# Performance work log

Measured on AMD Instinct MI355X. Metric: run time of the kernel, lower is better.

Reference implementation:

```python
import jax, jax.numpy as jnp
import numpy as np

VOCAB = 10000
EMB = 512
D_IMG = 2048
RNN = 1024
SEQ_LEN = 16
START_TOKEN = VOCAB + 1  # 10001
V_OUT = VOCAB + 3        # 10003


def setup_inputs() -> dict:
    key = jax.random.key(0)
    ks = jax.random.split(key, 24)
    g = lambda k, shape, fan_in: jax.random.normal(k, shape, jnp.float32) / np.sqrt(fan_in)
    inp = {
        "img_features": jax.random.normal(ks[0], (64, 196, D_IMG), jnp.float32),
        "captions": jax.random.randint(ks[1], (64, SEQ_LEN), 0, VOCAB),
        # embedding table
        "emb": g(ks[2], (V_OUT, EMB), EMB),
        # LSTMCell (PyTorch gate order i,f,g,o), stored as [in, 4H]
        "Wih": g(ks[3], (EMB + D_IMG, 4 * RNN), EMB + D_IMG),
        "Whh": g(ks[4], (RNN, 4 * RNN), RNN),
        "bih": jnp.zeros((4 * RNN,), jnp.float32),
        "bhh": jnp.zeros((4 * RNN,), jnp.float32),
        # init_h / init_c
        "Wh0": g(ks[5], (D_IMG, RNN), D_IMG), "bh0": jnp.zeros((RNN,), jnp.float32),
        "Wc0": g(ks[6], (D_IMG, RNN), D_IMG), "bc0": jnp.zeros((RNN,), jnp.float32),
        # f_beta gate
        "Wfb": g(ks[7], (RNN, D_IMG), RNN), "bfb": jnp.zeros((D_IMG,), jnp.float32),
        # deep_output
        "Wout": g(ks[8], (RNN, V_OUT), RNN), "bout": jnp.zeros((V_OUT,), jnp.float32),
        # attention: U (rnn->rnn), W (img->rnn), v (rnn->1)
        "WU": g(ks[9], (RNN, RNN), RNN), "bU": jnp.zeros((RNN,), jnp.float32),
        "WW": g(ks[10], (D_IMG, RNN), D_IMG), "bW": jnp.zeros((RNN,), jnp.float32),
        "Wv": g(ks[11], (RNN, 1), RNN), "bv": jnp.zeros((1,), jnp.float32),
    }
    return inp


def reference(img_features, captions, emb, Wih, Whh, bih, bhh, Wh0, bh0, Wc0, bc0,
              Wfb, bfb, Wout, bout, WU, bU, WW, bW, Wv, bv):
    B = img_features.shape[0]
    # get_target: prepend START token -> [B, T+1]
    start = jnp.full((B, 1), START_TOKEN, dtype=captions.dtype)
    target = jnp.concatenate([start, captions], axis=1)
    embedding = emb[target]                      # [B, T+1, EMB]
    emb_seq = jnp.transpose(embedding, (1, 0, 2))  # [T+1, B, EMB]

    # init LSTM state from mean image features
    avg = img_features.mean(axis=1)              # [B, D_IMG]
    h0 = jnp.tanh(avg @ Wh0 + bh0)
    c0 = jnp.tanh(avg @ Wc0 + bc0)

    # image-side attention projection is timestep-independent
    W_s = img_features @ WW + bW                 # [B, L, RNN]
    b_gates = bih + bhh

    def step(carry, emb_t):
        h, c = carry
        # additive attention
        U_h = h @ WU + bU                        # [B, RNN]
        att = jnp.tanh(W_s + U_h[:, None, :])    # [B, L, RNN]
        e = (att @ Wv).squeeze(-1) + bv          # [B, L]
        alpha = jax.nn.softmax(e, axis=1)
        context = jnp.einsum('bld,bl->bd', img_features, alpha)  # [B, D_IMG]
        gate = jax.nn.sigmoid(h @ Wfb + bfb)
        x = jnp.concatenate([emb_t, gate * context], axis=1)     # [B, EMB+D_IMG]
        # LSTMCell, PyTorch gate order i,f,g,o
        gates = x @ Wih + h @ Whh + b_gates      # [B, 4*RNN]
        i, f, gg, o = jnp.split(gates, 4, axis=1)
        c_new = jax.nn.sigmoid(f) * c + jax.nn.sigmoid(i) * jnp.tanh(gg)
        h_new = jax.nn.sigmoid(o) * jnp.tanh(c_new)
        out = h_new @ Wout + bout                # [B, V_OUT] (dropout=identity, eval mode)
        return (h_new, c_new), (out, alpha)

    (_, _), (preds_t, alphas_t) = jax.lax.scan(step, (h0, c0), emb_seq)
    preds = jnp.transpose(preds_t, (1, 0, 2))    # [B, T+1, V_OUT]
    alphas = jnp.transpose(alphas_t, (1, 0, 2))  # [B, T+1, L]
    return preds, alphas
```

## Files before the change

### kernel.cpp

```cpp
#include <hip/hip_runtime.h>
#include <cstdint>

#define NB    64
#define LIMG  196
#define DIMG  2048
#define RNND  1024
#define EMBD  512
#define TSTEPS 17
#define VOUTD 10003

typedef short bf16x8 __attribute__((ext_vector_type(8)));
typedef float f32x4  __attribute__((ext_vector_type(4)));

__device__ __forceinline__ float fast_sig(float x) {
    return 1.f / (1.f + __expf(-x));
}
__device__ __forceinline__ float fast_tanh(float x) {
    float ax = fabsf(x);
    float e  = __expf(2.f * ax);
    float r  = 1.f - 2.f / (e + 1.f);
    return copysignf(r, x);
}
__device__ __forceinline__ void split_bf(float x, short& hi, short& lo) {
    unsigned u  = __float_as_uint(x);
    unsigned hb = u & 0xffff0000u;
    hi = (short)(u >> 16);
    float r = x - __uint_as_float(hb);
    lo = (short)(__float_as_uint(r) >> 16);
}

__global__ __launch_bounds__(256) void tsplit(
    const float* __restrict__ S1, int ld1,
    const float* __restrict__ S2, int ld2,
    short* __restrict__ outh, short* __restrict__ outl,
    int N, int K, int ksplit, int nsplit)
{
    __shared__ float T[64][65];
    const int k0 = blockIdx.x * 64, n0 = blockIdx.y * 64;
    const int tid = threadIdx.x;
    const int rr = tid >> 2;
    const int cc = (tid & 3) * 16;
    const int kk = k0 + rr;
    const int nn = n0 + cc;
    const float* rp; int col;
    if (nsplit > 0) {
        if (nn >= nsplit) { rp = S2 + (size_t)kk * ld2; col = nn - nsplit; }
        else              { rp = S1 + (size_t)kk * ld1; col = nn; }
    } else {
        if (kk < ksplit)  { rp = S1 + (size_t)kk * ld1; col = nn; }
        else              { rp = S2 + (size_t)(kk - ksplit) * ld2; col = nn; }
    }
#pragma unroll
    for (int j = 0; j < 16; j++)
        T[rr][cc + j] = (nn + j < N) ? rp[col + j] : 0.f;
    __syncthreads();
    const int wn = tid >> 2;
    const int wk = (tid & 3) * 16;
    const int gn = n0 + wn;
    if (gn >= N) return;
    bf16x8 h0, h1, l0, l1;
#pragma unroll
    for (int j = 0; j < 8; j++) {
        short hh, ll;
        split_bf(T[wk + j][wn], hh, ll);     h0[j] = hh; l0[j] = ll;
        split_bf(T[wk + 8 + j][wn], hh, ll); h1[j] = hh; l1[j] = ll;
    }
    const size_t o = (size_t)gn * K + k0 + wk;
    *(bf16x8*)&outh[o]     = h0;
    *(bf16x8*)&outh[o + 8] = h1;
    *(bf16x8*)&outl[o]     = l0;
    *(bf16x8*)&outl[o + 8] = l1;
}

__global__ __launch_bounds__(256) void gemm_bb(
    const float* __restrict__ Af,
    const short* __restrict__ Ah16, const short* __restrict__ Al16,
    const short* __restrict__ Bh16, const short* __restrict__ Bl16,
    const float* __restrict__ bias, float* __restrict__ C,
    int M, int N, int K, int lda, int ldb, int ldc, int pmap)
{
    __shared__ short Ah[128 * 40], Al[128 * 40];
    __shared__ short Bh[128 * 40], Bl[128 * 40];

    const int tid = threadIdx.x;
    const int n0  = blockIdx.x * 128;
    const int m0  = blockIdx.y * 128;

    const int lane = tid & 63;
    const int w    = tid >> 6;
    const int wm   = (w >> 1) * 64;
    const int wn   = (w & 1) * 64;
    const int lm   = lane & 15;
    const int lk   = lane >> 4;

    const int ar = tid >> 1;
    const int ac = (tid & 1) * 16;

    f32x4 acc[4][4];
#pragma unroll
    for (int i = 0; i < 4; i++)
#pragma unroll
        for (int j = 0; j < 4; j++) acc[i][j] = (f32x4)0.f;

    for (int k0 = 0; k0 < K; k0 += 32) {
        bf16x8 ah0, ah1, al0, al1;
        if (Af) {
            float f[16];
            if (m0 + ar < M) {
                const float* ap = Af + (size_t)(m0 + ar) * lda + (k0 + ac);
                float4 q0 = *(const float4*)(ap);
                float4 q1 = *(const float4*)(ap + 4);
                float4 q2 = *(const float4*)(ap + 8);
                float4 q3 = *(const float4*)(ap + 12);
                f[0]=q0.x; f[1]=q0.y; f[2]=q0.z; f[3]=q0.w;
                f[4]=q1.x; f[5]=q1.y; f[6]=q1.z; f[7]=q1.w;
                f[8]=q2.x; f[9]=q2.y; f[10]=q2.z; f[11]=q2.w;
                f[12]=q3.x; f[13]=q3.y; f[14]=q3.z; f[15]=q3.w;
            } else {
#pragma unroll
                for (int j = 0; j < 16; j++) f[j] = 0.f;
            }
#pragma unroll
            for (int j = 0; j < 8; j++) {
                short hh, ll;
                split_bf(f[j], hh, ll);     ah0[j] = hh; al0[j] = ll;
                split_bf(f[8 + j], hh, ll); ah1[j] = hh; al1[j] = ll;
            }
        } else {
            const short* p = Ah16 + (size_t)(m0 + ar) * lda + (k0 + ac);
            ah0 = *(const bf16x8*)p; ah1 = *(const bf16x8*)(p + 8);
            const short* q = Al16 + (size_t)(m0 + ar) * lda + (k0 + ac);
            al0 = *(const bf16x8*)q; al1 = *(const bf16x8*)(q + 8);
        }
        const short* pb = Bh16 + (size_t)(n0 + ar) * ldb + (k0 + ac);
        bf16x8 bh0 = *(const bf16x8*)pb, bh1 = *(const bf16x8*)(pb + 8);
        const short* qb = Bl16 + (size_t)(n0 + ar) * ldb + (k0 + ac);
        bf16x8 bl0 = *(const bf16x8*)qb, bl1 = *(const bf16x8*)(qb + 8);

        __syncthreads();
        *(bf16x8*)&Ah[ar * 40 + ac]     = ah0;
        *(bf16x8*)&Ah[ar * 40 + ac + 8] = ah1;
        *(bf16x8*)&Al[ar * 40 + ac]     = al0;
        *(bf16x8*)&Al[ar * 40 + ac + 8] = al1;
        *(bf16x8*)&Bh[ar * 40 + ac]     = bh0;
        *(bf16x8*)&Bh[ar * 40 + ac + 8] = bh1;
        *(bf16x8*)&Bl[ar * 40 + ac]     = bl0;
        *(bf16x8*)&Bl[ar * 40 + ac + 8] = bl1;
        __syncthreads();

        bf16x8 afh[4], afl[4], bfh[4], bfl[4];
#pragma unroll
        for (int fm = 0; fm < 4; fm++) {
            const int idx = (wm + fm * 16 + lm) * 40 + lk * 8;
            afh[fm] = *(bf16x8*)&Ah[idx];
            afl[fm] = *(bf16x8*)&Al[idx];
        }
#pragma unroll
        for (int fn = 0; fn < 4; fn++) {
            const int idx = (wn + fn * 16 + lm) * 40 + lk * 8;
            bfh[fn] = *(bf16x8*)&Bh[idx];
            bfl[fn] = *(bf16x8*)&Bl[idx];
        }
#pragma unroll
        for (int fm = 0; fm < 4; fm++)
#pragma unroll
            for (int fn = 0; fn < 4; fn++) {
                acc[fm][fn] = __builtin_amdgcn_mfma_f32_16x16x32_bf16(afh[fm], bfh[fn], acc[fm][fn], 0, 0, 0);
                acc[fm][fn] = __builtin_amdgcn_mfma_f32_16x16x32_bf16(afh[fm], bfl[fn], acc[fm][fn], 0, 0, 0);
                acc[fm][fn] = __builtin_amdgcn_mfma_f32_16x16x32_bf16(afl[fm], bfh[fn], acc[fm][fn], 0, 0, 0);
            }
    }

#pragma unroll
    for (int fm = 0; fm < 4; fm++) {
#pragma unroll
        for (int fn = 0; fn < 4; fn++) {
            const int col = n0 + wn + fn * 16 + lm;
            if (col >= N) continue;
            const float bb = bias ? bias[col] : 0.f;
#pragma unroll
            for (int r = 0; r < 4; r++) {
                const int row = m0 + wm + fm * 16 + lk * 4 + r;
                if (row >= M) continue;
                const size_t orow = pmap ? (size_t)((row & 63) * TSTEPS + (row >> 6))
                                         : (size_t)row;
                C[orow * ldc + col] = acc[fm][fn][r] + bb;
            }
        }
    }
}

__global__ __launch_bounds__(256) void gemm_sk(
    const float* __restrict__ A,
    const short* __restrict__ Bh16, const short* __restrict__ Bl16,
    float* __restrict__ P, int N, int K, int lda, int ldb, int Kc)
{
    __shared__ short Ah[64 * 40], Al[64 * 40];
    __shared__ short Bh[128 * 40], Bl[128 * 40];

    const int tid = threadIdx.x;
    const int n0  = blockIdx.x * 128;
    const int s   = blockIdx.z;
    const int kb  = s * Kc;

    const int lane = tid & 63;
    const int w    = tid >> 6;
    const int wn   = w * 32;
    const int lm   = lane & 15;
    const int lk   = lane >> 4;

    const int a_r = tid >> 2;
    const int a_c = (tid & 3) * 8;
    const int b_r = tid >> 1;
    const int b_c = (tid & 1) * 16;

    f32x4 acc[4][2];
#pragma unroll
    for (int i = 0; i < 4; i++)
#pragma unroll
        for (int j = 0; j < 2; j++) acc[i][j] = (f32x4)0.f;

    for (int k0 = kb; k0 < kb + Kc; k0 += 32) {
        const float* ap = A + (size_t)a_r * lda + (k0 + a_c);
        float4 q0 = *(const float4*)(ap);
        float4 q1 = *(const float4*)(ap + 4);
        float f[8] = {q0.x, q0.y, q0.z, q0.w, q1.x, q1.y, q1.z, q1.w};
        bf16x8 ah, al;
#pragma unroll
        for (int j = 0; j < 8; j++) {
            short hh, ll;
            split_bf(f[j], hh, ll); ah[j] = hh; al[j] = ll;
        }
        const short* pb = Bh16 + (size_t)(n0 + b_r) * ldb + (k0 + b_c);
        bf16x8 bh0 = *(const bf16x8*)pb, bh1 = *(const bf16x8*)(pb + 8);
        const short* qb = Bl16 + (size_t)(n0 + b_r) * ldb + (k0 + b_c);
        bf16x8 bl0 = *(const bf16x8*)qb, bl1 = *(const bf16x8*)(qb + 8);

        __syncthreads();
        *(bf16x8*)&Ah[a_r * 40 + a_c] = ah;
        *(bf16x8*)&Al[a_r * 40 + a_c] = al;
        *(bf16x8*)&Bh[b_r * 40 + b_c]     = bh0;
        *(bf16x8*)&Bh[b_r * 40 + b_c + 8] = bh1;
        *(bf16x8*)&Bl[b_r * 40 + b_c]     = bl0;
        *(bf16x8*)&Bl[b_r * 40 + b_c + 8] = bl1;
        __syncthreads();

        bf16x8 afh[4], afl[4], bfh[2], bfl[2];
#pragma unroll
        for (int fm = 0; fm < 4; fm++) {
            const int idx = (fm * 16 + lm) * 40 + lk * 8;
            afh[fm] = *(bf16x8*)&Ah[idx];
            afl[fm] = *(bf16x8*)&Al[idx];
        }
#pragma unroll
        for (int fn = 0; fn < 2; fn++) {
            const int idx = (wn + fn * 16 + lm) * 40 + lk * 8;
            bfh[fn] = *(bf16x8*)&Bh[idx];
            bfl[fn] = *(bf16x8*)&Bl[idx];
        }
#pragma unroll
        for (int fm = 0; fm < 4; fm++)
#pragma unroll
            for (int fn = 0; fn < 2; fn++) {
                acc[fm][fn] = __builtin_amdgcn_mfma_f32_16x16x32_bf16(afh[fm], bfh[fn], acc[fm][fn], 0, 0, 0);
                acc[fm][fn] = __builtin_amdgcn_mfma_f32_16x16x32_bf16(afh[fm], bfl[fn], acc[fm][fn], 0, 0, 0);
                acc[fm][fn] = __builtin_amdgcn_mfma_f32_16x16x32_bf16(afl[fm], bfh[fn], acc[fm][fn], 0, 0, 0);
            }
    }

    float* Ps = P + (size_t)s * 64 * N;
#pragma unroll
    for (int fm = 0; fm < 4; fm++)
#pragma unroll
        for (int fn = 0; fn < 2; fn++) {
            const int col = n0 + wn + fn * 16 + lm;
#pragma unroll
            for (int r = 0; r < 4; r++) {
                const int row = fm * 16 + lk * 4 + r;
                Ps[(size_t)row * N + col] = acc[fm][fn][r];
            }
        }
}

__global__ __launch_bounds__(256) void gemm64(
    const float* __restrict__ A, const float* __restrict__ B,
    const float* __restrict__ bias, float* __restrict__ C,
    int N, int K, int Kc, int ldc, int act, int direct)
{
    __shared__ float As[16][64];
    __shared__ float Bs[16][68];

    const int tid = threadIdx.x;
    const int n0  = blockIdx.x * 64;
    const int m0  = blockIdx.y * 64;
    const int s   = blockIdx.z;
    const int kb  = s * Kc;
    const int ke  = min(K, kb + Kc);

    const int tm = (tid >> 4) << 2;
    const int tn = (tid & 15) << 2;

    float acc[4][4];
#pragma unroll
    for (int i = 0; i < 4; i++)
#pragma unroll
        for (int j = 0; j < 4; j++) acc[i][j] = 0.f;

    const int a_m = tid >> 2;
    const int a_k = (tid & 3) << 2;
    const int b_k = tid >> 4;
    const int b_n = (tid & 15) << 2;
    const bool n4 = ((N & 3) == 0);

    for (int k0 = kb; k0 < ke; k0 += 16) {
        float4 av = *(const float4*)(A + (size_t)(m0 + a_m) * K + (k0 + a_k));
        float4 bv;
        {
            const int nn = n0 + b_n;
            const float* brow = B + (size_t)(k0 + b_k) * N;
            if (n4) {
                bv = (nn < N) ? *(const float4*)(brow + nn) : make_float4(0.f,0.f,0.f,0.f);
            } else {
                bv.x = (nn + 0 < N) ? brow[nn + 0] : 0.f;
                bv.y = (nn + 1 < N) ? brow[nn + 1] : 0.f;
                bv.z = (nn + 2 < N) ? brow[nn + 2] : 0.f;
                bv.w = (nn + 3 < N) ? brow[nn + 3] : 0.f;
            }
        }
        __syncthreads();
        As[a_k + 0][a_m] = av.x;
        As[a_k + 1][a_m] = av.y;
        As[a_k + 2][a_m] = av.z;
        As[a_k + 3][a_m] = av.w;
        *(float4*)&Bs[b_k][b_n] = bv;
        __syncthreads();
#pragma unroll
        for (int k = 0; k < 16; k++) {
            float4 a4 = *(const float4*)&As[k][tm];
            float4 b4 = *(const float4*)&Bs[k][tn];
            acc[0][0] = fmaf(a4.x, b4.x, acc[0][0]);
            acc[0][1] = fmaf(a4.x, b4.y, acc[0][1]);
            acc[0][2] = fmaf(a4.x, b4.z, acc[0][2]);
            acc[0][3] = fmaf(a4.x, b4.w, acc[0][3]);
            acc[1][0] = fmaf(a4.y, b4.x, acc[1][0]);
            acc[1][1] = fmaf(a4.y, b4.y, acc[1][1]);
            acc[1][2] = fmaf(a4.y, b4.z, acc[1][2]);
            acc[1][3] = fmaf(a4.y, b4.w, acc[1][3]);
            acc[2][0] = fmaf(a4.z, b4.x, acc[2][0]);
            acc[2][1] = fmaf(a4.z, b4.y, acc[2][1]);
            acc[2][2] = fmaf(a4.z, b4.z, acc[2][2]);
            acc[2][3] = fmaf(a4.z, b4.w, acc[2][3]);
            acc[3][0] = fmaf(a4.w, b4.x, acc[3][0]);
            acc[3][1] = fmaf(a4.w, b4.y, acc[3][1]);
            acc[3][2] = fmaf(a4.w, b4.z, acc[3][2]);
            acc[3][3] = fmaf(a4.w, b4.w, acc[3][3]);
        }
    }

    if (direct) {
#pragma unroll
        for (int i = 0; i < 4; i++) {
            const int m = m0 + tm + i;
            const size_t row = (size_t)m * ldc;
#pragma unroll
            for (int j = 0; j < 4; j++) {
                const int n = n0 + tn + j;
                if (n < N) {
                    float v = acc[i][j] + (bias ? bias[n] : 0.f);
                    if (act == 1) v = fast_tanh(v);
                    else if (act == 2) v = fast_sig(v);
                    C[row + n] = v;
                }
            }
        }
    } else {
        float* Pp = C + (size_t)s * 64 * N;
#pragma unroll
        for (int i = 0; i < 4; i++) {
#pragma unroll
            for (int j = 0; j < 4; j++) {
                const int n = n0 + tn + j;
                if (n < N) Pp[(size_t)(tm + i) * N + n] = acc[i][j];
            }
        }
    }
}

__global__ __launch_bounds__(256) void gemm_mfma3(
    const float* __restrict__ A, const float* __restrict__ B,
    const float* __restrict__ bias, float* __restrict__ C,
    int M, int N, int K, int lda, int ldb, int ldc, int pmap)
{
    __shared__ short Ah[128 * 40], Al[128 * 40];
    __shared__ short Bh[128 * 40], Bl[128 * 40];

    const int tid = threadIdx.x;
    const int n0  = blockIdx.x * 128;
    const int m0  = blockIdx.y * 128;

    const int lane = tid & 63;
    const int w    = tid >> 6;
    const int wm   = (w >> 1) * 64;
    const int wn   = (w & 1) * 64;
    const int lm   = lane & 15;
    const int lk   = lane >> 4;

    const int ar = tid >> 1;
    const int ac = (tid & 1) * 16;
    const int kb = (tid & 15) * 2;
    const int c8 = (tid >> 4) * 8;

    const bool bvec = ((ldb & 3) == 0) && (n0 + 128 <= N);

    f32x4 acc[4][4];
#pragma unroll
    for (int i = 0; i < 4; i++)
#pragma unroll
        for (int j = 0; j < 4; j++) acc[i][j] = (f32x4)0.f;

    for (int k0 = 0; k0 < K; k0 += 32) {
        float f[16];
        if (m0 + ar < M) {
            const float* ap = A + (size_t)(m0 + ar) * lda + (k0 + ac);
            float4 q0 = *(const float4*)(ap);
            float4 q1 = *(const float4*)(ap + 4);
            float4 q2 = *(const float4*)(ap + 8);
            float4 q3 = *(const float4*)(ap + 12);
            f[0]=q0.x; f[1]=q0.y; f[2]=q0.z; f[3]=q0.w;
            f[4]=q1.x; f[5]=q1.y; f[6]=q1.z; f[7]=q1.w;
            f[8]=q2.x; f[9]=q2.y; f[10]=q2.z; f[11]=q2.w;
            f[12]=q3.x; f[13]=q3.y; f[14]=q3.z; f[15]=q3.w;
        } else {
#pragma unroll
            for (int j = 0; j < 16; j++) f[j] = 0.f;
        }
        bf16x8 h0, h1, l0, l1;
#pragma unroll
        for (int j = 0; j < 8; j++) {
            short hh, ll;
            split_bf(f[j], hh, ll);     h0[j] = hh; l0[j] = ll;
            split_bf(f[8 + j], hh, ll); h1[j] = hh; l1[j] = ll;
        }
        float g0[8], g1[8];
        if (bvec) {
            const float* bp0 = B + (size_t)(k0 + kb) * ldb + (n0 + c8);
            const float* bp1 = bp0 + ldb;
            float4 q0 = *(const float4*)(bp0);
            float4 q1 = *(const float4*)(bp0 + 4);
            float4 q2 = *(const float4*)(bp1);
            float4 q3 = *(const float4*)(bp1 + 4);
            g0[0]=q0.x; g0[1]=q0.y; g0[2]=q0.z; g0[3]=q0.w;
            g0[4]=q1.x; g0[5]=q1.y; g0[6]=q1.z; g0[7]=q1.w;
            g1[0]=q2.x; g1[1]=q2.y; g1[2]=q2.z; g1[3]=q2.w;
            g1[4]=q3.x; g1[5]=q3.y; g1[6]=q3.z; g1[7]=q3.w;
        } else {
            const float* bp0 = B + (size_t)(k0 + kb) * ldb;
            const float* bp1 = bp0 + ldb;
#pragma unroll
            for (int j = 0; j < 8; j++) {
                const int nn = n0 + c8 + j;
                g0[j] = (nn < N) ? bp0[nn] : 0.f;
                g1[j] = (nn < N) ? bp1[nn] : 0.f;
            }
        }
        __syncthreads();
        *(bf16x8*)&Ah[ar * 40 + ac]     = h0;
        *(bf16x8*)&Ah[ar * 40 + ac + 8] = h1;
        *(bf16x8*)&Al[ar * 40 + ac]     = l0;
        *(bf16x8*)&Al[ar * 40 + ac + 8] = l1;
#pragma unroll
        for (int j = 0; j < 8; j++) {
            short ha, la, hb, lb;
            split_bf(g0[j], ha, la);
            split_bf(g1[j], hb, lb);
            const int ci = (c8 + j) * 40 + kb;
            *(int*)&Bh[ci] = (int)((unsigned short)ha | ((unsigned)(unsigned short)hb << 16));
            *(int*)&Bl[ci] = (int)((unsigned short)la | ((unsigned)(unsigned short)lb << 16));
        }
        __syncthreads();

        bf16x8 afh[4], afl[4], bfh[4], bfl[4];
#pragma unroll
        for (int fm = 0; fm < 4; fm++) {
            const int idx = (wm + fm * 16 + lm) * 40 + lk * 8;
            afh[fm] = *(bf16x8*)&Ah[idx];
            afl[fm] = *(bf16x8*)&Al[idx];
        }
#pragma unroll
        for (int fn = 0; fn < 4; fn++) {
            const int idx = (wn + fn * 16 + lm) * 40 + lk * 8;
            bfh[fn] = *(bf16x8*)&Bh[idx];
            bfl[fn] = *(bf16x8*)&Bl[idx];
        }
#pragma unroll
        for (int fm = 0; fm < 4; fm++)
#pragma unroll
            for (int fn = 0; fn < 4; fn++) {
                acc[fm][fn] = __builtin_amdgcn_mfma_f32_16x16x32_bf16(afh[fm], bfh[fn], acc[fm][fn], 0, 0, 0);
                acc[fm][fn] = __builtin_amdgcn_mfma_f32_16x16x32_bf16(afh[fm], bfl[fn], acc[fm][fn], 0, 0, 0);
                acc[fm][fn] = __builtin_amdgcn_mfma_f32_16x16x32_bf16(afl[fm], bfh[fn], acc[fm][fn], 0, 0, 0);
            }
    }

#pragma unroll
    for (int fm = 0; fm < 4; fm++) {
#pragma unroll
        for (int fn = 0; fn < 4; fn++) {
            const int col = n0 + wn + fn * 16 + lm;
            if (col >= N) continue;
            const float bb = bias ? bias[col] : 0.f;
#pragma unroll
            for (int r = 0; r < 4; r++) {
                const int row = m0 + wm + fm * 16 + lk * 4 + r;
                if (row >= M) continue;
                const size_t orow = pmap ? (size_t)((row & 63) * TSTEPS + (row >> 6))
                                         : (size_t)row;
                C[orow * ldc + col] = acc[fm][fn][r] + bb;
            }
        }
    }
}

__global__ __launch_bounds__(256) void reduce_partials(
    const float* __restrict__ P, int S, int N,
    const float* __restrict__ bias, float* __restrict__ C, int ldc, int act)
{
    const int idx = blockIdx.x * 256 + threadIdx.x;
    const int total = 64 * N;
    if (idx >= total) return;
    const int m = idx / N;
    const int n = idx - m * N;
    float v = bias ? bias[n] : 0.f;
    for (int s = 0; s < S; s++) v += P[(size_t)s * total + idx];
    if (act == 1) v = fast_tanh(v);
    else if (act == 2) v = fast_sig(v);
    else if (act == 3 && n >= RNND) v = fast_sig(v);
    C[(size_t)m * ldc + n] = v;
}

__global__ __launch_bounds__(256) void reduce_lstm(
    const float* __restrict__ P, int S, const float* __restrict__ bsum,
    float* __restrict__ hn, float* __restrict__ c,
    short* __restrict__ hbh, short* __restrict__ hbl)
{
    const int idx = blockIdx.x * 256 + threadIdx.x;
    const int b = idx >> 10, r = idx & 1023;
    const float* pb = P + (size_t)b * 4096;
    float gi = bsum[r], gf = bsum[1024 + r], gg = bsum[2048 + r], go = bsum[3072 + r];
    for (int s = 0; s < S; s++) {
        const float* q = pb + (size_t)s * 64 * 4096;
        gi += q[r]; gf += q[1024 + r]; gg += q[2048 + r]; go += q[3072 + r];
    }
    const float ig = fast_sig(gi);
    const float fg = fast_sig(gf);
    const float g2 = fast_tanh(gg);
    const float og = fast_sig(go);
    const float cn = fg * c[idx] + ig * g2;
    const float hv = og * fast_tanh(cn);
    c[idx]  = cn;
    hn[idx] = hv;
    if (hbh) {
        short hi, lo;
        split_bf(hv, hi, lo);
        hbh[idx] = hi;
        hbl[idx] = lo;
    }
}

__global__ __launch_bounds__(256) void mean_img(
    const float* __restrict__ img, float* __restrict__ avg)
{
    const int b = blockIdx.x;
    const int d = blockIdx.y * 256 + threadIdx.x;
    const float* p = img + (size_t)b * LIMG * DIMG + d;
    float s = 0.f;
    for (int l = 0; l < LIMG; l++) s += p[(size_t)l * DIMG];
    avg[(size_t)b * DIMG + d] = s * (1.f / 196.f);
}

__global__ __launch_bounds__(256) void concat_w(
    const float* __restrict__ WU, const float* __restrict__ Wfb,
    float* __restrict__ Wug)
{
    const int idx = blockIdx.x * 256 + threadIdx.x;
    if (idx >= 1024 * 3072) return;
    const int k = idx / 3072;
    const int j = idx - k * 3072;
    Wug[idx] = (j < 1024) ? WU[(size_t)k * 1024 + j] : Wfb[(size_t)k * 2048 + (j - 1024)];
}

__global__ __launch_bounds__(256) void concat_b(
    const float* __restrict__ bU, const float* __restrict__ bfb,
    const float* __restrict__ bih, const float* __restrict__ bhh,
    float* __restrict__ bug, float* __restrict__ bsum)
{
    const int j = blockIdx.x * 256 + threadIdx.x;
    if (j < 3072) bug[j] = (j < 1024) ? bU[j] : bfb[j - 1024];
    if (j < 4096) bsum[j] = bih[j] + bhh[j];
}

__global__ __launch_bounds__(256) void attn_e(
    const float* __restrict__ Ws, const float* __restrict__ ug,
    const float* __restrict__ Wv, const float* __restrict__ bv,
    float* __restrict__ e)
{
    const int wv   = (blockIdx.x << 2) + (threadIdx.x >> 6);
    const int lane = threadIdx.x & 63;
    const int b    = wv / LIMG;
    const float* wrow = Ws + (size_t)wv * RNND;
    const float* urow = ug + (size_t)b * 3072;
    float acc = 0.f;
#pragma unroll
    for (int k = lane * 4; k < RNND; k += 256) {
        float4 wq = *(const float4*)(wrow + k);
        float4 uq = *(const float4*)(urow + k);
        float4 vq = *(const float4*)(Wv + k);
        acc += fast_tanh(wq.x + uq.x) * vq.x + fast_tanh(wq.y + uq.y) * vq.y
             + fast_tanh(wq.z + uq.z) * vq.z + fast_tanh(wq.w + uq.w) * vq.w;
    }
#pragma unroll
    for (int off = 32; off > 0; off >>= 1) acc += __shfl_down(acc, off);
    if (lane == 0) e[wv] = acc + bv[0];
}

__global__ __launch_bounds__(256) void softmax_alpha(
    const float* __restrict__ e, float* __restrict__ alpha,
    float* __restrict__ alphas_out, int t)
{
    __shared__ float red[256];
    const int b = blockIdx.x, tid = threadIdx.x;
    const float v = (tid < LIMG) ? e[b * LIMG + tid] : -3.0e38f;
    red[tid] = v; __syncthreads();
    for (int s = 128; s > 0; s >>= 1) {
        if (tid < s) red[tid] = fmaxf(red[tid], red[tid + s]);
        __syncthreads();
    }
    const float mx = red[0]; __syncthreads();
    const float ex = (tid < LIMG) ? __expf(v - mx) : 0.f;
    red[tid] = ex; __syncthreads();
    for (int s = 128; s > 0; s >>= 1) {
        if (tid < s) red[tid] += red[tid + s];
        __syncthreads();
    }
    const float inv = 1.f / red[0];
    if (tid < LIMG) {
        const float a = ex * inv;
        alpha[b * LIMG + tid] = a;
        alphas_out[(size_t)b * (TSTEPS * LIMG) + t * LIMG + tid] = a;
    }
}

__global__ __launch_bounds__(128) void assemble_x(
    const float* __restrict__ img, const float* __restrict__ alpha,
    const float* __restrict__ ug, const float* __restrict__ emb,
    const int* __restrict__ captions, const float* __restrict__ h,
    float* __restrict__ x, int t, int stride)
{
    const int b = blockIdx.x, y = blockIdx.y, tid = threadIdx.x;
    if (y < 4) {
        const int tok = (t == 0) ? 10001 : captions[b * 16 + (t - 1)];
        const int j = y * 128 + tid;
        x[(size_t)b * stride + j] = emb[(size_t)tok * EMBD + j];
    } else if (y < 20) {
        __shared__ float al[LIMG];
        for (int i = tid; i < LIMG; i += 128) al[i] = alpha[b * LIMG + i];
        __syncthreads();
        const int d = (y - 4) * 128 + tid;
        const float* ib = img + (size_t)b * LIMG * DIMG + d;
        float accv = 0.f;
#pragma unroll 4
        for (int l = 0; l < LIMG; l++) accv = fmaf(al[l], ib[(size_t)l * DIMG], accv);
        const float g = ug[(size_t)b * 3072 + 1024 + d];
        x[(size_t)b * stride + EMBD + d] = g * accv;
    } else {
        const int j = (y - 20) * 128 + tid;
        x[(size_t)b * stride + 2560 + j] = h[(size_t)b * RNND + j];
    }
}

extern "C" void kernel_launch(void* const* d_in, const int* in_sizes, int n_in,
                              void* d_out, int out_size, void* d_ws, size_t ws_size,
                              hipStream_t stream)
{
    const float* img      = (const float*)d_in[0];
    const int*   captions = (const int*)d_in[1];
    const float* emb      = (const float*)d_in[2];
    const float* Wih      = (const float*)d_in[3];
    const float* Whh      = (const float*)d_in[4];
    const float* bih      = (const float*)d_in[5];
    const float* bhh      = (const float*)d_in[6];
    const float* Wh0      = (const float*)d_in[7];
    const float* bh0      = (const float*)d_in[8];
    const float* Wc0      = (const float*)d_in[9];
    const float* bc0      = (const float*)d_in[10];
    const float* Wfb      = (const float*)d_in[11];
    const float* bfb      = (const float*)d_in[12];
    const float* Wout     = (const float*)d_in[13];
    const float* bout     = (const float*)d_in[14];
    const float* WU       = (const float*)d_in[15];
    const float* bU       = (const float*)d_in[16];
    const float* WW       = (const float*)d_in[17];
    const float* bW       = (const float*)d_in[18];
    const float* Wv       = (const float*)d_in[19];
    const float* bv       = (const float*)d_in[20];

    float* preds      = (float*)d_out;
    float* alphas_out = preds + (size_t)NB * TSTEPS * VOUTD;

    const size_t NEED = 190000000;

    if (ws_size >= NEED) {
        float* w = (float*)d_ws;
        float* Ws    = w; w += (size_t)12544 * 1024;
        float* ug    = w; w += (size_t)64 * 3072;
        float* P     = w; w += (size_t)8 * 64 * 4096;
        float* e     = w; w += (size_t)64 * LIMG;
        float* alpha = w; w += (size_t)64 * LIMG;
        float* xh    = w; w += (size_t)64 * 3584;
        float* h     = w; w += (size_t)64 * RNND;
        float* c     = w; w += (size_t)64 * RNND;
        float* avg   = w; w += (size_t)64 * DIMG;
        float* bsum  = w; w += 4096;
        float* bug   = w; w += 3072;
        short* u = (short*)w;
        short* Hbh     = u; u += (size_t)1280 * 1024;
        short* Hbl     = u; u += (size_t)1280 * 1024;
        short* WWTh    = u; u += (size_t)1024 * 2048;
        short* WWTl    = u; u += (size_t)1024 * 2048;
        short* WugTh   = u; u += (size_t)3072 * 1024;
        short* WugTl   = u; u += (size_t)3072 * 1024;
        short* WfullTh = u; u += (size_t)4096 * 3584;
        short* WfullTl = u; u += (size_t)4096 * 3584;
        short* WoutTh  = u; u += (size_t)10112 * 1024;
        short* WoutTl  = u; u += (size_t)10112 * 1024;

        mean_img<<<dim3(NB, 8), 256, 0, stream>>>(img, avg);
        gemm64<<<dim3(16, 1, 8), 256, 0, stream>>>(avg, Wh0, nullptr, P, 1024, 2048, 256, 0, 0, 0);
        reduce_partials<<<256, 256, 0, stream>>>(P, 8, 1024, bh0, h, 1024, 1);
        gemm64<<<dim3(16, 1, 8), 256, 0, stream>>>(avg, Wc0, nullptr, P, 1024, 2048, 256, 0, 0, 0);
        reduce_partials<<<256, 256, 0, stream>>>(P, 8, 1024, bc0, c, 1024, 1);
        concat_b<<<16, 256, 0, stream>>>(bU, bfb, bih, bhh, bug, bsum);

        tsplit<<<dim3(32, 16), 256, 0, stream>>>(WW, 1024, WW, 1024, WWTh, WWTl, 1024, 2048, 2048, 0);
        tsplit<<<dim3(16, 48), 256, 0, stream>>>(WU, 1024, Wfb, 2048, WugTh, WugTl, 3072, 1024, 1024, 1024);
        tsplit<<<dim3(56, 64), 256, 0, stream>>>(Wih, 4096, Whh, 4096, WfullTh, WfullTl, 4096, 3584, 2560, 0);
        tsplit<<<dim3(16, 157), 256, 0, stream>>>(Wout, VOUTD, Wout, VOUTD, WoutTh, WoutTl, VOUTD, 1024, 1024, 0);

        gemm_bb<<<dim3(8, 98), 256, 0, stream>>>(img, nullptr, nullptr, WWTh, WWTl,
                                                 bW, Ws, 12544, 1024, 2048, 2048, 2048, 1024, 0);

        for (int t = 0; t < TSTEPS; t++) {
            gemm_sk<<<dim3(24, 1, 8), 256, 0, stream>>>(h, WugTh, WugTl, P, 3072, 1024, 1024, 1024, 128);
            reduce_partials<<<768, 256, 0, stream>>>(P, 8, 3072, bug, ug, 3072, 3);
            attn_e<<<3136, 256, 0, stream>>>(Ws, ug, Wv, bv, e);
            softmax_alpha<<<NB, 256, 0, stream>>>(e, alpha, alphas_out, t);
            assemble_x<<<dim3(NB, 28), 128, 0, stream>>>(img, alpha, ug, emb, captions, h, xh, t, 3584);
            gemm_sk<<<dim3(32, 1, 7), 256, 0, stream>>>(xh, WfullTh, WfullTl, P, 4096, 3584, 3584, 3584, 512);
            reduce_lstm<<<256, 256, 0, stream>>>(P, 7, bsum, h, c,
                                                 Hbh + (size_t)(t + 1) * 65536,
                                                 Hbl + (size_t)(t + 1) * 65536);
        }

        gemm_bb<<<dim3(79, 9), 256, 0, stream>>>(nullptr, Hbh + 65536, Hbl + 65536,
                                                 WoutTh, WoutTl, bout, preds,
                                                 1088, VOUTD, 1024, 1024, 1024, VOUTD, 1);
    } else {
        float* w = (float*)d_ws;
        float* Ws    = w; w += (size_t)12544 * 1024;
        float* ug    = w; w += (size_t)64 * 3072;
        float* P     = w; w += (size_t)12 * 64 * 4096;
        float* e     = w; w += (size_t)64 * LIMG;
        float* alpha = w; w += (size_t)64 * LIMG;
        float* x     = w; w += (size_t)64 * 2560;
        float* Hh    = w; w += (size_t)18 * 64 * RNND;
        float* c     = w; w += (size_t)64 * RNND;
        float* avg   = w; w += (size_t)64 * DIMG;
        float* bsum  = w; w += 4096;
        float* Wug   = w; w += (size_t)1024 * 3072;
        float* bug   = w; w += 3072;

        mean_img<<<dim3(NB, 8), 256, 0, stream>>>(img, avg);
        gemm64<<<dim3(16, 1, 8), 256, 0, stream>>>(avg, Wh0, nullptr, P, 1024, 2048, 256, 0, 0, 0);
        reduce_partials<<<256, 256, 0, stream>>>(P, 8, 1024, bh0, Hh, 1024, 1);
        gemm64<<<dim3(16, 1, 8), 256, 0, stream>>>(avg, Wc0, nullptr, P, 1024, 2048, 256, 0, 0, 0);
        reduce_partials<<<256, 256, 0, stream>>>(P, 8, 1024, bc0, c, 1024, 1);
        concat_b<<<16, 256, 0, stream>>>(bU, bfb, bih, bhh, bug, bsum);
        concat_w<<<12288, 256, 0, stream>>>(WU, Wfb, Wug);
        gemm_mfma3<<<dim3(8, 98), 256, 0, stream>>>(img, WW, bW, Ws,
                                                    12544, 1024, 2048, 2048, 1024, 1024, 0);
        for (int t = 0; t < TSTEPS; t++) {
            const float* h  = Hh + (size_t)t * 64 * RNND;
            float*       hn = Hh + (size_t)(t + 1) * 64 * RNND;
            gemm64<<<dim3(48, 1, 8), 256, 0, stream>>>(h, Wug, nullptr, P, 3072, 1024, 128, 0, 0, 0);
            reduce_partials<<<768, 256, 0, stream>>>(P, 8, 3072, bug, ug, 3072, 3);
            attn_e<<<3136, 256, 0, stream>>>(Ws, ug, Wv, bv, e);
            softmax_alpha<<<NB, 256, 0, stream>>>(e, alpha, alphas_out, t);
            assemble_x<<<dim3(NB, 20), 128, 0, stream>>>(img, alpha, ug, emb, captions, h, x, t, 2560);
            gemm64<<<dim3(64, 1, 8), 256, 0, stream>>>(x, Wih, nullptr, P, 4096, 2560, 320, 0, 0, 0);
            gemm64<<<dim3(64, 1, 4), 256, 0, stream>>>(h, Whh, nullptr, P + (size_t)8 * 64 * 4096,
                                                       4096, 1024, 256, 0, 0, 0);
            reduce_lstm<<<256, 256, 0, stream>>>(P, 12, bsum, hn, c, nullptr, nullptr);
        }
        gemm_mfma3<<<dim3(79, 9), 256, 0, stream>>>(Hh + (size_t)64 * RNND, Wout, bout, preds,
                                                    TSTEPS * 64, VOUTD, 1024, 1024, VOUTD, VOUTD, 1);
    }
}
```

Before: 1.828 ms.

## Fuse softmax with context assembly and remap GEMM blocks per XCD

Merges the per-step softmax_alpha and assemble_x kernels into a single ctx_fuse kernel. Each block recomputes the softmax over 196 positions, then either writes alphas, the embedding and h, or computes a 512-wide slice of the gated context. This removes one launch per timestep. The bf16-split GEMM now takes a 1D grid that is remapped so contiguous tile groups land on the same XCD, aiming for better L2 reuse. The cost is redundant softmax work in every block and a lower-parallelism context kernel (5x64 blocks of 256 threads, versus 28x64 blocks of 128 before).

```diff
diff --git a/kernel.cpp b/kernel.cpp
--- a/kernel.cpp
+++ b/kernel.cpp
@@ -77,15 +77,27 @@
     const short* __restrict__ Ah16, const short* __restrict__ Al16,
     const short* __restrict__ Bh16, const short* __restrict__ Bl16,
     const float* __restrict__ bias, float* __restrict__ C,
-    int M, int N, int K, int lda, int ldb, int ldc, int pmap)
+    int M, int N, int K, int lda, int ldb, int ldc, int pmap,
+    int nx, int ny, int gax)
 {
     __shared__ short Ah[128 * 40], Al[128 * 40];
     __shared__ short Bh[128 * 40], Bl[128 * 40];
 
+    const int p    = blockIdx.x;
+    const int xcd  = p & 7;
+    const int slot = p >> 3;
+    const int G = gax ? ny : nx;
+    const int O = gax ? nx : ny;
+    const int qb = G >> 3, qr = G & 7;
+    const int cnt = qb + (xcd < qr ? 1 : 0);
+    if (slot >= cnt * O) return;
+    const int start = xcd * qb + min(xcd, qr);
+    const int g = start + slot / O;
+    const int o = slot - (slot / O) * O;
+    const int n0 = (gax ? o : g) * 128;
+    const int m0 = (gax ? g : o) * 128;
+
     const int tid = threadIdx.x;
-    const int n0  = blockIdx.x * 128;
-    const int m0  = blockIdx.y * 128;
-
     const int lane = tid & 63;
     const int w    = tid >> 6;
     const int wm   = (w >> 1) * 64;
@@ -127,15 +139,15 @@
                 split_bf(f[8 + j], hh, ll); ah1[j] = hh; al1[j] = ll;
             }
         } else {
-            const short* p = Ah16 + (size_t)(m0 + ar) * lda + (k0 + ac);
-            ah0 = *(const bf16x8*)p; ah1 = *(const bf16x8*)(p + 8);
-            const short* q = Al16 + (size_t)(m0 + ar) * lda + (k0 + ac);
-            al0 = *(const bf16x8*)q; al1 = *(const bf16x8*)(q + 8);
+            const short* pa = Ah16 + (size_t)(m0 + ar) * lda + (k0 + ac);
+            ah0 = *(const bf16x8*)pa; ah1 = *(const bf16x8*)(pa + 8);
+            const short* qa = Al16 + (size_t)(m0 + ar) * lda + (k0 + ac);
+            al0 = *(const bf16x8*)qa; al1 = *(const bf16x8*)(qa + 8);
         }
         const short* pb = Bh16 + (size_t)(n0 + ar) * ldb + (k0 + ac);
         bf16x8 bh0 = *(const bf16x8*)pb, bh1 = *(const bf16x8*)(pb + 8);
-        const short* qb = Bl16 + (size_t)(n0 + ar) * ldb + (k0 + ac);
-        bf16x8 bl0 = *(const bf16x8*)qb, bl1 = *(const bf16x8*)(qb + 8);
+        const short* qb2 = Bl16 + (size_t)(n0 + ar) * ldb + (k0 + ac);
+        bf16x8 bl0 = *(const bf16x8*)qb2, bl1 = *(const bf16x8*)(qb2 + 8);
 
         __syncthreads();
         *(bf16x8*)&Ah[ar * 40 + ac]     = ah0;
@@ -621,6 +633,58 @@
 #pragma unroll
     for (int off = 32; off > 0; off >>= 1) acc += __shfl_down(acc, off);
     if (lane == 0) e[wv] = acc + bv[0];
+}
+
+__global__ __launch_bounds__(256) void ctx_fuse(
+    const float* __restrict__ e, const float* __restrict__ img,
+    const float* __restrict__ ug, const float* __restrict__ embt,
+    const int* __restrict__ captions, const float* __restrict__ h,
+    float* __restrict__ x, float* __restrict__ alphas_out, int t)
+{
+    __shared__ float al[256];
+    __shared__ float red[256];
+    const int b = blockIdx.x, y = blockIdx.y, tid = threadIdx.x;
+
+    const float v = (tid < LIMG) ? e[b * LIMG + tid] : -3.0e38f;
+    red[tid] = v; __syncthreads();
+    for (int s = 128; s > 0; s >>= 1) {
+        if (tid < s) red[tid] = fmaxf(red[tid], red[tid + s]);
+        __syncthreads();
+    }
+    const float mx = red[0]; __syncthreads();
+    const float ex = (tid < LIMG) ? __expf(v - mx) : 0.f;
+    red[tid] = ex; __syncthreads();
+    for (int s = 128; s > 0; s >>= 1) {
+        if (tid < s) red[tid] += red[tid + s];
+        __syncthreads();
+    }
+    const float inv = 1.f / red[0];
+    al[tid] = ex * inv;
+    __syncthreads();
+
+    if (y == 0) {
+        if (tid < LIMG)
+            alphas_out[(size_t)b * (TSTEPS * LIMG) + t * LIMG + tid] = al[tid];
+        const int tok = (t == 0) ? 10001 : captions[b * 16 + (t - 1)];
+        for (int j = tid; j < EMBD; j += 256)
+            x[(size_t)b * 3584 + j] = embt[(size_t)tok * EMBD + j];
+        for (int j = tid; j < RNND; j += 256)
+            x[(size_t)b * 3584 + 2560 + j] = h[(size_t)b * RNND + j];
+    } else {
+        const int d0 = (y - 1) * 512 + tid * 2;
+        const float* ib = img + (size_t)b * LIMG * DIMG + d0;
+        float a0 = 0.f, a1 = 0.f;
+#pragma unroll 4
+        for (int l = 0; l < LIMG; l++) {
+            float2 q = *(const float2*)(ib + (size_t)l * DIMG);
+            a0 = fmaf(al[l], q.x, a0);
+            a1 = fmaf(al[l], q.y, a1);
+        }
+        const float g0 = ug[(size_t)b * 3072 + 1024 + d0];
+        const float g1 = ug[(size_t)b * 3072 + 1024 + d0 + 1];
+        x[(size_t)b * 3584 + EMBD + d0]     = g0 * a0;
+        x[(size_t)b * 3584 + EMBD + d0 + 1] = g1 * a1;
+    }
 }
 
 __global__ __launch_bounds__(256) void softmax_alpha(
@@ -746,24 +810,25 @@
         tsplit<<<dim3(56, 64), 256, 0, stream>>>(Wih, 4096, Whh, 4096, WfullTh, WfullTl, 4096, 3584, 2560, 0);
         tsplit<<<dim3(16, 157), 256, 0, stream>>>(Wout, VOUTD, Wout, VOUTD, WoutTh, WoutTl, VOUTD, 1024, 1024, 0);
 
-        gemm_bb<<<dim3(8, 98), 256, 0, stream>>>(img, nullptr, nullptr, WWTh, WWTl,
-                                                 bW, Ws, 12544, 1024, 2048, 2048, 2048, 1024, 0);
+        gemm_bb<<<832, 256, 0, stream>>>(img, nullptr, nullptr, WWTh, WWTl,
+                                         bW, Ws, 12544, 1024, 2048, 2048, 2048, 1024, 0,
+                                         8, 98, 1);
 
         for (int t = 0; t < TSTEPS; t++) {
             gemm_sk<<<dim3(24, 1, 8), 256, 0, stream>>>(h, WugTh, WugTl, P, 3072, 1024, 1024, 1024, 128);
             reduce_partials<<<768, 256, 0, stream>>>(P, 8, 3072, bug, ug, 3072, 3);
             attn_e<<<3136, 256, 0, stream>>>(Ws, ug, Wv, bv, e);
-            softmax_alpha<<<NB, 256, 0, stream>>>(e, alpha, alphas_out, t);
-            assemble_x<<<dim3(NB, 28), 128, 0, stream>>>(img, alpha, ug, emb, captions, h, xh, t, 3584);
+            ctx_fuse<<<dim3(NB, 5), 256, 0, stream>>>(e, img, ug, emb, captions, h, xh, alphas_out, t);
             gemm_sk<<<dim3(32, 1, 7), 256, 0, stream>>>(xh, WfullTh, WfullTl, P, 4096, 3584, 3584, 3584, 512);
             reduce_lstm<<<256, 256, 0, stream>>>(P, 7, bsum, h, c,
                                                  Hbh + (size_t)(t + 1) * 65536,
                                                  Hbl + (size_t)(t + 1) * 65536);
         }
 
-        gemm_bb<<<dim3(79, 9), 256, 0, stream>>>(nullptr, Hbh + 65536, Hbl + 65536,
-                                                 WoutTh, WoutTl, bout, preds,
-                                                 1088, VOUTD, 1024, 1024, 1024, VOUTD, 1);
+        gemm_bb<<<720, 256, 0, stream>>>(nullptr, Hbh + 65536, Hbl + 65536,
+                                         WoutTh, WoutTl, bout, preds,
+                                         1088, VOUTD, 1024, 1024, 1024, VOUTD, 1,
+                                         79, 9, 0);
     } else {
         float* w = (float*)d_ws;
         float* Ws    = w; w += (size_t)12544 * 1024;
@@ -789,15 +854,15 @@
         gemm_mfma3<<<dim3(8, 98), 256, 0, stream>>>(img, WW, bW, Ws,
                                                     12544, 1024, 2048, 2048, 1024, 1024, 0);
         for (int t = 0; t < TSTEPS; t++) {
-            const float* h  = Hh + (size_t)t * 64 * RNND;
+            const float* hc = Hh + (size_t)t * 64 * RNND;
             float*       hn = Hh + (size_t)(t + 1) * 64 * RNND;
-            gemm64<<<dim3(48, 1, 8), 256, 0, stream>>>(h, Wug, nullptr, P, 3072, 1024, 128, 0, 0, 0);
+            gemm64<<<dim3(48, 1, 8), 256, 0, stream>>>(hc, Wug, nullptr, P, 3072, 1024, 128, 0, 0, 0);
             reduce_partials<<<768, 256, 0, stream>>>(P, 8, 3072, bug, ug, 3072, 3);
             attn_e<<<3136, 256, 0, stream>>>(Ws, ug, Wv, bv, e);
             softmax_alpha<<<NB, 256, 0, stream>>>(e, alpha, alphas_out, t);
-            assemble_x<<<dim3(NB, 20), 128, 0, stream>>>(img, alpha, ug, emb, captions, h, x, t, 2560);
+            assemble_x<<<dim3(NB, 20), 128, 0, stream>>>(img, alpha, ug, emb, captions, hc, x, t, 2560);
             gemm64<<<dim3(64, 1, 8), 256, 0, stream>>>(x, Wih, nullptr, P, 4096, 2560, 320, 0, 0, 0);
-            gemm64<<<dim3(64, 1, 4), 256, 0, stream>>>(h, Whh, nullptr, P + (size_t)8 * 64 * 4096,
+            gemm64<<<dim3(64, 1, 4), 256, 0, stream>>>(hc, Whh, nullptr, P + (size_t)8 * 64 * 4096,
                                                        4096, 1024, 256, 0, 0, 0);
             reduce_lstm<<<256, 256, 0, stream>>>(P, 12, bsum, hn, c, nullptr, nullptr);
         }
```

After: 1.769 ms. -3.2%, faster.
